# Optimization experiments

Hardware: AMD Instinct MI355X
Metric: run time of the kernel (lower is better)

The kernel has to match this reference:

```python
import jax, jax.numpy as jnp
import numpy as np

HIDDEN = 4096
N_HEADS = 32
N_KV_HEADS = 8
HEAD_DIM = 128
ROPE_BASE = 10000.0


def setup_inputs() -> dict:
    key = jax.random.key(0)
    k1, k2, k3, k4, k5 = jax.random.split(key, 5)
    s = 0.02  # init scale for weights
    return {
        "hidden_states": jax.random.normal(k1, (1, 2048, HIDDEN), dtype=jnp.float32),
        "Wq": jax.random.normal(k2, (N_HEADS * HEAD_DIM, HIDDEN), dtype=jnp.float32) * s,
        "Wk": jax.random.normal(k3, (N_KV_HEADS * HEAD_DIM, HIDDEN), dtype=jnp.float32) * s,
        "Wv": jax.random.normal(k4, (N_KV_HEADS * HEAD_DIM, HIDDEN), dtype=jnp.float32) * s,
        "Wo": jax.random.normal(k5, (HIDDEN, HIDDEN), dtype=jnp.float32) * s,
    }


def _rope(x, cos, sin):
    # x: [B, H, T, D]; cos/sin: [T, D/2] -> rotate split halves (Llama style)
    d2 = x.shape[-1] // 2
    x1, x2 = x[..., :d2], x[..., d2:]
    return jnp.concatenate([x1 * cos - x2 * sin, x1 * sin + x2 * cos], axis=-1)


def reference(hidden_states, Wq, Wk, Wv, Wo):
    B, T, _ = hidden_states.shape
    H, Hkv, D = N_HEADS, N_KV_HEADS, HEAD_DIM
    G = H // Hkv  # kv groups

    q = jnp.einsum("bth,qh->btq", hidden_states, Wq).reshape(B, T, H, D).transpose(0, 2, 1, 3)
    k = jnp.einsum("bth,kh->btk", hidden_states, Wk).reshape(B, T, Hkv, D).transpose(0, 2, 1, 3)
    v = jnp.einsum("bth,vh->btv", hidden_states, Wv).reshape(B, T, Hkv, D).transpose(0, 2, 1, 3)

    # RoPE (position_offset = 0)
    positions = jnp.arange(T, dtype=jnp.float32)
    inv_freq = ROPE_BASE ** (-jnp.arange(0, D, 2, dtype=jnp.float32) / D)  # [D/2]
    angles = positions[:, None] * inv_freq[None, :]                        # [T, D/2]
    cos, sin = jnp.cos(angles), jnp.sin(angles)
    q = _rope(q, cos, sin)
    k = _rope(k, cos, sin)

    # GQA attention without materializing expanded K/V: group query heads
    qg = q.reshape(B, Hkv, G, T, D)
    scale = 1.0 / jnp.sqrt(jnp.asarray(D, dtype=q.dtype))
    scores = jnp.einsum("bkgtd,bksd->bkgts", qg, k) * scale  # [B, Hkv, G, T, T]
    causal = jnp.tril(jnp.ones((T, T), dtype=bool))
    scores = jnp.where(causal, scores, jnp.finfo(scores.dtype).min)
    probs = jax.nn.softmax(scores, axis=-1)
    attn = jnp.einsum("bkgts,bksd->bkgtd", probs, v)          # [B, Hkv, G, T, D]
    attn = attn.reshape(B, H, T, D).transpose(0, 2, 1, 3).reshape(B, T, H * D)

    return jnp.einsum("btq,oq->bto", attn, Wo)
```

## Files before the change

### kernel.cpp

```cpp
#include <hip/hip_runtime.h>
#include <stdint.h>

#define T_SEQ   2048
#define HID     4096
#define NH      32
#define NKV     8
#define HD      128
#define QCOLS   6144
#define QK_SCALE 0.08838834764831845f

typedef _Float16 half_t;
typedef _Float16 half8 __attribute__((ext_vector_type(8)));
typedef _Float16 half4v __attribute__((ext_vector_type(4)));
typedef float    f32x4 __attribute__((ext_vector_type(4)));

typedef __attribute__((address_space(1))) const void cg_void;
typedef __attribute__((address_space(3))) void lds_void;

__global__ __launch_bounds__(256) void cast_all_k(const float* __restrict__ X,
                                                  const float* __restrict__ Wq,
                                                  const float* __restrict__ Wk,
                                                  const float* __restrict__ Wv,
                                                  const float* __restrict__ Wo,
                                                  half_t* __restrict__ Xh,
                                                  half_t* __restrict__ Wqkvh,
                                                  half_t* __restrict__ Woh) {
  int i = blockIdx.x * 256 + threadIdx.x;
  const float* src; half_t* dst; int off;
  if (i < 2097152)      { src = X;  dst = Xh;               off = i; }
  else if (i < 6291456) { src = Wq; dst = Wqkvh;            off = i - 2097152; }
  else if (i < 7340032) { src = Wk; dst = Wqkvh + 16777216; off = i - 6291456; }
  else if (i < 8388608) { src = Wv; dst = Wqkvh + 20971520; off = i - 7340032; }
  else                  { src = Wo; dst = Woh;              off = i - 8388608; }
  f32x4 v = *(const f32x4*)(src + (size_t)off * 4);
  half4v o;
  o[0] = (half_t)v[0]; o[1] = (half_t)v[1]; o[2] = (half_t)v[2]; o[3] = (half_t)v[3];
  *(half4v*)(dst + (size_t)off * 4) = o;
}

__global__ __launch_bounds__(256) void rope_tables_k(float* __restrict__ cs) {
  int idx = blockIdx.x * 256 + threadIdx.x;
  int t = idx >> 6, i = idx & 63;
  float inv = expf(-(float)i * 0.14391156831212787f);
  float a = (float)t * inv;
  cs[idx] = cosf(a);
  cs[131072 + idx] = sinf(a);
}

__global__ __launch_bounds__(256) void rope_vt_k(half_t* __restrict__ QKV,
                                                 const float* __restrict__ cs,
                                                 half_t* __restrict__ Vt) {
  if (blockIdx.x < 20480) {
    int idx = blockIdx.x * 256 + threadIdx.x;
    int i = idx & 63;
    int rem = idx >> 6;
    int head = rem % 40;
    int t = rem / 40;
    int colbase = (head < 32) ? head * HD : HID + (head - 32) * HD;
    size_t base = (size_t)t * QCOLS + colbase;
    float c = cs[t * 64 + i], s = cs[131072 + t * 64 + i];
    float x1 = (float)QKV[base + i];
    float x2 = (float)QKV[base + 64 + i];
    float o1 = x1 * c - x2 * s;
    float o2 = x1 * s + x2 * c;
    if (head < 32) { o1 *= QK_SCALE; o2 *= QK_SCALE; }
    QKV[base + i]      = (half_t)o1;
    QKV[base + 64 + i] = (half_t)o2;
  } else {
    int idx = (blockIdx.x - 20480) * 256 + threadIdx.x;
    int d  = idx & 127;
    int ts = (idx >> 7) & 255;
    int kh = idx >> 15;
    half8 o;
#pragma unroll
    for (int i = 0; i < 8; ++i)
      o[i] = QKV[(size_t)(ts * 8 + i) * QCOLS + HID + NKV * HD + kh * HD + d];
    *(half8*)&Vt[(size_t)kh * (HD * T_SEQ) + (size_t)d * T_SEQ + ts * 8] = o;
  }
}

template <int BM, int BN, int OUT_HALF>
__global__ __launch_bounds__(512, 2) void gemm8p_k(const half_t* __restrict__ A,
                                                   const half_t* __restrict__ Bm,
                                                   void* __restrict__ Cout,
                                                   int M, int N, int K) {
  constexpr int MF = BM / 32;
  constexpr int NF = BN / 64;
  constexpr int MH = MF / 2;
  constexpr int LA = BM / 64;
  constexpr int LB = BN / 64;
  __shared__ half_t Al[2][BM * 64];
  __shared__ half_t Bl[2][BN * 64];

  const int nbm = M / BM;
  const int nwg = nbm * (N / BN);
  const int bid = blockIdx.x;
  const int swz = (bid & 7) * (nwg >> 3) + (bid >> 3);
  const int brow = (swz % nbm) * BM;
  const int bcol = (swz / nbm) * BN;
  const int tid = threadIdx.x;
  const int lane = tid & 63, wid = tid >> 6;
  const int wr = wid >> 2, wc = wid & 3;
  const int lr = lane & 15, hi = lane >> 4;
  const int wrow = wr * (MF * 16), wcol = wc * (NF * 16);

  const half_t* Ab = A + (size_t)brow * K;
  const half_t* Bb = Bm + (size_t)bcol * K;

  f32x4 acc[MF][NF] = {};
  half8 afr[MH], bfr[NF];

#define STAGE_A(l, k0, buf) { \
    int c_ = (l) * 512 + tid; int r_ = c_ >> 3, s_ = c_ & 7; \
    __builtin_amdgcn_global_load_lds( \
      (cg_void*)(Ab + (size_t)r_ * K + (k0) + ((s_ ^ (r_ & 7)) * 8)), \
      (lds_void*)(&Al[buf][((l) * 512 + wid * 64) * 8]), 16, 0, 0); }
#define STAGE_B(l, k0, buf) { \
    int c_ = (l) * 512 + tid; int r_ = c_ >> 3, s_ = c_ & 7; \
    __builtin_amdgcn_global_load_lds( \
      (cg_void*)(Bb + (size_t)r_ * K + (k0) + ((s_ ^ (r_ & 7)) * 8)), \
      (lds_void*)(&Bl[buf][((l) * 512 + wid * 64) * 8]), 16, 0, 0); }
#define RD_A(i, mh, kk, buf) { \
    int row_ = wrow + ((mh) * MH + (i)) * 16 + lr; int ks_ = (kk) * 4 + hi; \
    afr[i] = *(const half8*)&Al[buf][row_ * 64 + ((ks_ ^ (row_ & 7)) * 8)]; }
#define RD_B(n, kk, buf) { \
    int row_ = wcol + (n) * 16 + lr; int ks_ = (kk) * 4 + hi; \
    bfr[n] = *(const half8*)&Bl[buf][row_ * 64 + ((ks_ ^ (row_ & 7)) * 8)]; }
#define MFMA_PH(mh) { \
    __builtin_amdgcn_s_setprio(1); \
    _Pragma("unroll") for (int i_ = 0; i_ < MH; ++i_) \
      _Pragma("unroll") for (int n_ = 0; n_ < NF; ++n_) \
        acc[(mh) * MH + i_][n_] = __builtin_amdgcn_mfma_f32_16x16x32_f16( \
            afr[i_], bfr[n_], acc[(mh) * MH + i_][n_], 0, 0, 0); \
    __builtin_amdgcn_s_setprio(0); }

#define DO_TILE(T, BUF) { \
    const int kn_ = ((T) + 1) * 64; const bool pf_ = ((T) + 1) < NT; \
    if (pf_) { _Pragma("unroll") for (int l_ = 0; l_ < LA; ++l_) STAGE_A(l_, kn_, (BUF) ^ 1); } \
    _Pragma("unroll") for (int n_ = 0; n_ < NF; ++n_) RD_B(n_, 0, BUF); \
    _Pragma("unroll") for (int i_ = 0; i_ < MH; ++i_) RD_A(i_, 0, 0, BUF); \
    MFMA_PH(0); \
    __builtin_amdgcn_s_barrier(); __builtin_amdgcn_sched_barrier(0); \
    if (pf_) { _Pragma("unroll") for (int l_ = 0; l_ < LB; ++l_) STAGE_B(l_, kn_, (BUF) ^ 1); } \
    _Pragma("unroll") for (int i_ = 0; i_ < MH; ++i_) RD_A(i_, 1, 0, BUF); \
    MFMA_PH(1); \
    __builtin_amdgcn_s_barrier(); __builtin_amdgcn_sched_barrier(0); \
    _Pragma("unroll") for (int n_ = 0; n_ < NF; ++n_) RD_B(n_, 1, BUF); \
    _Pragma("unroll") for (int i_ = 0; i_ < MH; ++i_) RD_A(i_, 1, 1, BUF); \
    MFMA_PH(1); \
    __builtin_amdgcn_s_barrier(); __builtin_amdgcn_sched_barrier(0); \
    _Pragma("unroll") for (int i_ = 0; i_ < MH; ++i_) RD_A(i_, 0, 1, BUF); \
    MFMA_PH(0); \
    asm volatile("s_waitcnt vmcnt(0)" ::: "memory"); \
    __syncthreads(); }

  const int NT = K / 64;
#pragma unroll
  for (int l_ = 0; l_ < LA; ++l_) STAGE_A(l_, 0, 0);
#pragma unroll
  for (int l_ = 0; l_ < LB; ++l_) STAGE_B(l_, 0, 0);
  asm volatile("s_waitcnt vmcnt(0)" ::: "memory");
  __syncthreads();

  for (int t = 0; t < NT; t += 2) {
    DO_TILE(t, 0);
    DO_TILE(t + 1, 1);
  }

#undef STAGE_A
#undef STAGE_B
#undef RD_A
#undef RD_B
#undef MFMA_PH
#undef DO_TILE

#pragma unroll
  for (int m = 0; m < MF; ++m)
#pragma unroll
    for (int n = 0; n < NF; ++n)
#pragma unroll
      for (int r = 0; r < 4; ++r) {
        int row = brow + wrow + m * 16 + hi * 4 + r;
        int col = bcol + wcol + n * 16 + lr;
        float v = acc[m][n][r];
        if (OUT_HALF) ((half_t*)Cout)[(size_t)row * N + col] = (half_t)v;
        else          ((float*)Cout)[(size_t)row * N + col] = v;
      }
}

__global__ __launch_bounds__(256, 2) void attn_k(const half_t* __restrict__ QKV,
                                                 const half_t* __restrict__ Vt,
                                                 half_t* __restrict__ Ob) {
  const int bid = blockIdx.x;
  const int qb = 31 - (bid >> 5);
  const int h  = bid & 31;
  const int kh = h >> 2;
  const int tid = threadIdx.x;
  const int lane = tid & 63;
  const int w = tid >> 6;
  const int lr = lane & 15, hi = lane >> 4;
  const int qrow = qb * 64 + w * 16;

  __shared__ half_t Klds[2][64 * 128];
  __shared__ half_t Vlds[2][128 * 64];
  __shared__ half_t Plds[4 * 16 * 72];

  const half_t* Qp  = QKV + h * HD;
  const half_t* Kp  = QKV + HID + kh * HD;
  const half_t* Vtp = Vt + (size_t)kh * (HD * T_SEQ);

  half8 qf[4];
#pragma unroll
  for (int kk = 0; kk < 4; ++kk)
    qf[kk] = *(const half8*)&Qp[(size_t)(qrow + lr) * QCOLS + kk * 32 + hi * 8];

  f32x4 acc[8] = {};
  float mrow[4], lrow[4];
#pragma unroll
  for (int r = 0; r < 4; ++r) { mrow[r] = -1e30f; lrow[r] = 0.0f; }

  half_t* Pw = &Plds[w * (16 * 72)];

#define STAGE_KV(kv0, buf) { \
    _Pragma("unroll") for (int c_ = 0; c_ < 4; ++c_) { \
      int chunk_ = c_ * 256 + tid; \
      int r_ = chunk_ >> 4, s_ = chunk_ & 15; \
      int cc_ = (s_ & 8) | ((s_ ^ r_) & 7); \
      __builtin_amdgcn_global_load_lds( \
          (cg_void*)(Kp + (size_t)((kv0) + r_) * QCOLS + cc_ * 8), \
          (lds_void*)(&Klds[buf][(c_ * 256 + w * 64) * 8]), 16, 0, 0); } \
    _Pragma("unroll") for (int c_ = 0; c_ < 4; ++c_) { \
      int chunk_ = c_ * 256 + tid; \
      int r_ = chunk_ >> 3, s_ = chunk_ & 7; \
      int cc_ = (s_ ^ r_) & 7; \
      __builtin_amdgcn_global_load_lds( \
          (cg_void*)(Vtp + (size_t)r_ * T_SEQ + (kv0) + cc_ * 8), \
          (lds_void*)(&Vlds[buf][(c_ * 256 + w * 64) * 8]), 16, 0, 0); } }

#define COMPUTE(T, BUF) { \
    const int kv0_ = (T) * 64; \
    f32x4 sc[4] = {}; \
    _Pragma("unroll") for (int jt_ = 0; jt_ < 4; ++jt_) \
      _Pragma("unroll") for (int kk_ = 0; kk_ < 4; ++kk_) { \
        int srow_ = jt_ * 16 + lr; \
        int sl_ = kk_ * 4 + hi; \
        int c_ = (sl_ & 8) | ((sl_ ^ srow_) & 7); \
        half8 kf_ = *(const half8*)&Klds[BUF][srow_ * 128 + c_ * 8]; \
        sc[jt_] = __builtin_amdgcn_mfma_f32_16x16x32_f16(qf[kk_], kf_, sc[jt_], 0, 0, 0); \
      } \
    if ((T) == qb) { \
      _Pragma("unroll") for (int jt_ = 0; jt_ < 4; ++jt_) \
        _Pragma("unroll") for (int r_ = 0; r_ < 4; ++r_) { \
          int ig_ = qrow + hi * 4 + r_; \
          int jg_ = kv0_ + jt_ * 16 + lr; \
          if (jg_ > ig_) sc[jt_][r_] = -1e30f; \
        } \
    } \
    float mx_[4]; \
    _Pragma("unroll") for (int r_ = 0; r_ < 4; ++r_) \
      mx_[r_] = fmaxf(fmaxf(sc[0][r_], sc[1][r_]), fmaxf(sc[2][r_], sc[3][r_])); \
    _Pragma("unroll") for (int off_ = 1; off_ < 16; off_ <<= 1) \
      _Pragma("unroll") for (int r_ = 0; r_ < 4; ++r_) \
        mx_[r_] = fmaxf(mx_[r_], __shfl_xor(mx_[r_], off_, 64)); \
    bool grow_ = false; \
    _Pragma("unroll") for (int r_ = 0; r_ < 4; ++r_) grow_ = grow_ || (mx_[r_] > mrow[r_]); \
    if (__any(grow_)) { \
      float scl_[4]; \
      _Pragma("unroll") for (int r_ = 0; r_ < 4; ++r_) { \
        float mn_ = fmaxf(mrow[r_], mx_[r_]); \
        scl_[r_] = __expf(mrow[r_] - mn_); \
        mrow[r_] = mn_; \
        float ls_ = 0.0f; \
        _Pragma("unroll") for (int jt_ = 0; jt_ < 4; ++jt_) { \
          sc[jt_][r_] = __expf(sc[jt_][r_] - mn_); ls_ += sc[jt_][r_]; } \
        lrow[r_] = lrow[r_] * scl_[r_] + ls_; \
      } \
      _Pragma("unroll") for (int g_ = 0; g_ < 8; ++g_) \
        _Pragma("unroll") for (int r_ = 0; r_ < 4; ++r_) acc[g_][r_] *= scl_[r_]; \
    } else { \
      _Pragma("unroll") for (int r_ = 0; r_ < 4; ++r_) { \
        float ls_ = 0.0f; \
        _Pragma("unroll") for (int jt_ = 0; jt_ < 4; ++jt_) { \
          sc[jt_][r_] = __expf(sc[jt_][r_] - mrow[r_]); ls_ += sc[jt_][r_]; } \
        lrow[r_] += ls_; \
      } \
    } \
    _Pragma("unroll") for (int jt_ = 0; jt_ < 4; ++jt_) \
      _Pragma("unroll") for (int r_ = 0; r_ < 4; ++r_) \
        Pw[(hi * 4 + r_) * 72 + jt_ * 16 + lr] = (half_t)sc[jt_][r_]; \
    half8 pf0_ = *(const half8*)&Pw[lr * 72 + hi * 8]; \
    half8 pf1_ = *(const half8*)&Pw[lr * 72 + 32 + hi * 8]; \
    _Pragma("unroll") for (int g_ = 0; g_ < 8; ++g_) { \
      int vrow_ = g_ * 16 + lr; \
      { int c0_ = (hi ^ vrow_) & 7; \
        half8 vf_ = *(const half8*)&Vlds[BUF][vrow_ * 64 + c0_ * 8]; \
        acc[g_] = __builtin_amdgcn_mfma_f32_16x16x32_f16(pf0_, vf_, acc[g_], 0, 0, 0); } \
      { int c1_ = ((4 + hi) ^ vrow_) & 7; \
        half8 vf_ = *(const half8*)&Vlds[BUF][vrow_ * 64 + c1_ * 8]; \
        acc[g_] = __builtin_amdgcn_mfma_f32_16x16x32_f16(pf1_, vf_, acc[g_], 0, 0, 0); } \
    } }

#define TILE_SYNC() { asm volatile("s_waitcnt vmcnt(0)" ::: "memory"); \
                      __builtin_amdgcn_s_barrier(); __builtin_amdgcn_sched_barrier(0); }

  const int nt = qb + 1;
  STAGE_KV(0, 0);
  TILE_SYNC();

  int t = 0;
  for (; t + 2 <= nt; t += 2) {
    STAGE_KV((t + 1) * 64, 1);
    COMPUTE(t, 0);
    TILE_SYNC();
    if (t + 2 < nt) { STAGE_KV((t + 2) * 64, 0); }
    COMPUTE(t + 1, 1);
    TILE_SYNC();
  }
  if (t < nt) { COMPUTE(t, 0); }

#undef STAGE_KV
#undef COMPUTE
#undef TILE_SYNC

  float linv[4];
#pragma unroll
  for (int r = 0; r < 4; ++r) {
    float l = lrow[r];
#pragma unroll
    for (int off = 1; off < 16; off <<= 1) l += __shfl_xor(l, off, 64);
    linv[r] = 1.0f / l;
  }
#pragma unroll
  for (int g = 0; g < 8; ++g)
#pragma unroll
    for (int r = 0; r < 4; ++r) {
      int row = qrow + hi * 4 + r;
      int col = h * HD + g * 16 + lr;
      Ob[(size_t)row * HID + col] = (half_t)(acc[g][r] * linv[r]);
    }
}

extern "C" void kernel_launch(void* const* d_in, const int* in_sizes, int n_in,
                              void* d_out, int out_size, void* d_ws, size_t ws_size,
                              hipStream_t stream) {
  const float* hs = (const float*)d_in[0];
  const float* Wq = (const float*)d_in[1];
  const float* Wk = (const float*)d_in[2];
  const float* Wv = (const float*)d_in[3];
  const float* Wo = (const float*)d_in[4];
  float* out = (float*)d_out;

  char* ws = (char*)d_ws;
  half_t* Xh    = (half_t*)(ws + 0);
  half_t* Vt    = (half_t*)(ws + 0);
  half_t* Wqkvh = (half_t*)(ws + 16777216);
  half_t* Woh   = (half_t*)(ws + 67108864);
  half_t* QKV   = (half_t*)(ws + 100663296);
  half_t* attnh = (half_t*)(ws + 125829120);
  float*  cs    = (float*)(ws + 142606336);
  if (ws_size < 143654912ull) return;

  cast_all_k<<<49152, 256, 0, stream>>>(hs, Wq, Wk, Wv, Wo, Xh, Wqkvh, Woh);
  rope_tables_k<<<512, 256, 0, stream>>>(cs);

  gemm8p_k<256, 192, 1><<<256, 512, 0, stream>>>(Xh, Wqkvh, (void*)QKV, 2048, 6144, 4096);
  rope_vt_k<<<21504, 256, 0, stream>>>(QKV, cs, Vt);
  attn_k<<<1024, 256, 0, stream>>>(QKV, Vt, attnh);
  gemm8p_k<128, 256, 0><<<256, 512, 0, stream>>>(attnh, Woh, (void*)out, 2048, 4096, 4096);
}
```

Baseline: 323.1 us.

## Switch projection GEMMs to 32x32x16 MFMA with new LDS swizzle

Rewrites both projection GEMMs to use 32x32x16 f16 MFMA tiles with configurable wave layout (WM x WN), instead of 16x16x32 tiles. The LDS swizzle is changed to XOR in extra row bits so that the 32-lane-row fragment reads avoid bank conflicts. Larger MFMA tiles need fewer LDS fragment reads per FLOP and fewer instructions. The cost is a larger accumulator register footprint per wave, which could hurt occupancy at 512 threads with two blocks per CU, and a more scattered epilogue store pattern.

Result: slower. 332.3 us (+2.9%).

```diff
diff --git a/kernel.cpp b/kernel.cpp
--- a/kernel.cpp
+++ b/kernel.cpp
@@ -13,6 +13,7 @@
 typedef _Float16 half8 __attribute__((ext_vector_type(8)));
 typedef _Float16 half4v __attribute__((ext_vector_type(4)));
 typedef float    f32x4 __attribute__((ext_vector_type(4)));
+typedef float    f32x16 __attribute__((ext_vector_type(16)));
 
 typedef __attribute__((address_space(1))) const void cg_void;
 typedef __attribute__((address_space(3))) void lds_void;
@@ -79,14 +80,15 @@
   }
 }
 
-template <int BM, int BN, int OUT_HALF>
-__global__ __launch_bounds__(512, 2) void gemm8p_k(const half_t* __restrict__ A,
+#define SWZF(row) (((row) & 7) ^ ((((row) >> 3) & 3) << 1))
+
+template <int BM, int BN, int WM, int WN, int OUT_HALF>
+__global__ __launch_bounds__(512, 2) void gemm32_k(const half_t* __restrict__ A,
                                                    const half_t* __restrict__ Bm,
                                                    void* __restrict__ Cout,
                                                    int M, int N, int K) {
-  constexpr int MF = BM / 32;
-  constexpr int NF = BN / 64;
-  constexpr int MH = MF / 2;
+  constexpr int MR = BM / (WM * 32);
+  constexpr int NR = BN / (WN * 32);
   constexpr int LA = BM / 64;
   constexpr int LB = BN / 64;
   __shared__ half_t Al[2][BM * 64];
@@ -100,57 +102,62 @@
   const int bcol = (swz / nbm) * BN;
   const int tid = threadIdx.x;
   const int lane = tid & 63, wid = tid >> 6;
-  const int wr = wid >> 2, wc = wid & 3;
-  const int lr = lane & 15, hi = lane >> 4;
-  const int wrow = wr * (MF * 16), wcol = wc * (NF * 16);
+  const int wr = wid / WN, wc = wid % WN;
+  const int l32 = lane & 31, h32 = lane >> 5;
+  const int wrow = wr * (MR * 32), wcol = wc * (NR * 32);
 
   const half_t* Ab = A + (size_t)brow * K;
   const half_t* Bb = Bm + (size_t)bcol * K;
 
-  f32x4 acc[MF][NF] = {};
-  half8 afr[MH], bfr[NF];
+  f32x16 acc[MR][NR] = {};
+  half8 afr[MR], bfr[NR];
 
 #define STAGE_A(l, k0, buf) { \
     int c_ = (l) * 512 + tid; int r_ = c_ >> 3, s_ = c_ & 7; \
     __builtin_amdgcn_global_load_lds( \
-      (cg_void*)(Ab + (size_t)r_ * K + (k0) + ((s_ ^ (r_ & 7)) * 8)), \
+      (cg_void*)(Ab + (size_t)r_ * K + (k0) + ((s_ ^ SWZF(r_)) * 8)), \
       (lds_void*)(&Al[buf][((l) * 512 + wid * 64) * 8]), 16, 0, 0); }
 #define STAGE_B(l, k0, buf) { \
     int c_ = (l) * 512 + tid; int r_ = c_ >> 3, s_ = c_ & 7; \
     __builtin_amdgcn_global_load_lds( \
-      (cg_void*)(Bb + (size_t)r_ * K + (k0) + ((s_ ^ (r_ & 7)) * 8)), \
+      (cg_void*)(Bb + (size_t)r_ * K + (k0) + ((s_ ^ SWZF(r_)) * 8)), \
       (lds_void*)(&Bl[buf][((l) * 512 + wid * 64) * 8]), 16, 0, 0); }
-#define RD_A(i, mh, kk, buf) { \
-    int row_ = wrow + ((mh) * MH + (i)) * 16 + lr; int ks_ = (kk) * 4 + hi; \
-    afr[i] = *(const half8*)&Al[buf][row_ * 64 + ((ks_ ^ (row_ & 7)) * 8)]; }
+#define RD_A(m, kk, buf) { \
+    int row_ = wrow + (m) * 32 + l32; int sl_ = ((kk) * 2 + h32) ^ SWZF(row_); \
+    afr[m] = *(const half8*)&Al[buf][row_ * 64 + sl_ * 8]; }
 #define RD_B(n, kk, buf) { \
-    int row_ = wcol + (n) * 16 + lr; int ks_ = (kk) * 4 + hi; \
-    bfr[n] = *(const half8*)&Bl[buf][row_ * 64 + ((ks_ ^ (row_ & 7)) * 8)]; }
-#define MFMA_PH(mh) { \
+    int row_ = wcol + (n) * 32 + l32; int sl_ = ((kk) * 2 + h32) ^ SWZF(row_); \
+    bfr[n] = *(const half8*)&Bl[buf][row_ * 64 + sl_ * 8]; }
+#define MFMA_K() { \
     __builtin_amdgcn_s_setprio(1); \
-    _Pragma("unroll") for (int i_ = 0; i_ < MH; ++i_) \
-      _Pragma("unroll") for (int n_ = 0; n_ < NF; ++n_) \
-        acc[(mh) * MH + i_][n_] = __builtin_amdgcn_mfma_f32_16x16x32_f16( \
-            afr[i_], bfr[n_], acc[(mh) * MH + i_][n_], 0, 0, 0); \
+    _Pragma("unroll") for (int m_ = 0; m_ < MR; ++m_) \
+      _Pragma("unroll") for (int n_ = 0; n_ < NR; ++n_) \
+        acc[m_][n_] = __builtin_amdgcn_mfma_f32_32x32x16_f16( \
+            afr[m_], bfr[n_], acc[m_][n_], 0, 0, 0); \
     __builtin_amdgcn_s_setprio(0); }
+#define RD_ALL(kk, buf) { \
+    _Pragma("unroll") for (int n_ = 0; n_ < NR; ++n_) RD_B(n_, kk, buf); \
+    _Pragma("unroll") for (int m_ = 0; m_ < MR; ++m_) RD_A(m_, kk, buf); }
 
 #define DO_TILE(T, BUF) { \
     const int kn_ = ((T) + 1) * 64; const bool pf_ = ((T) + 1) < NT; \
+     \
     if (pf_) { _Pragma("unroll") for (int l_ = 0; l_ < LA; ++l_) STAGE_A(l_, kn_, (BUF) ^ 1); } \
-    _Pragma("unroll") for (int n_ = 0; n_ < NF; ++n_) RD_B(n_, 0, BUF); \
-    _Pragma("unroll") for (int i_ = 0; i_ < MH; ++i_) RD_A(i_, 0, 0, BUF); \
-    MFMA_PH(0); \
+    RD_ALL(0, BUF); \
+    MFMA_K(); \
     __builtin_amdgcn_s_barrier(); __builtin_amdgcn_sched_barrier(0); \
+     \
     if (pf_) { _Pragma("unroll") for (int l_ = 0; l_ < LB; ++l_) STAGE_B(l_, kn_, (BUF) ^ 1); } \
-    _Pragma("unroll") for (int i_ = 0; i_ < MH; ++i_) RD_A(i_, 1, 0, BUF); \
-    MFMA_PH(1); \
+    RD_ALL(1, BUF); \
+    MFMA_K(); \
     __builtin_amdgcn_s_barrier(); __builtin_amdgcn_sched_barrier(0); \
-    _Pragma("unroll") for (int n_ = 0; n_ < NF; ++n_) RD_B(n_, 1, BUF); \
-    _Pragma("unroll") for (int i_ = 0; i_ < MH; ++i_) RD_A(i_, 1, 1, BUF); \
-    MFMA_PH(1); \
+     \
+    RD_ALL(2, BUF); \
+    MFMA_K(); \
     __builtin_amdgcn_s_barrier(); __builtin_amdgcn_sched_barrier(0); \
-    _Pragma("unroll") for (int i_ = 0; i_ < MH; ++i_) RD_A(i_, 0, 1, BUF); \
-    MFMA_PH(0); \
+     \
+    RD_ALL(3, BUF); \
+    MFMA_K(); \
     asm volatile("s_waitcnt vmcnt(0)" ::: "memory"); \
     __syncthreads(); }
 
@@ -171,17 +178,18 @@
 #undef STAGE_B
 #undef RD_A
 #undef RD_B
-#undef MFMA_PH
+#undef RD_ALL
+#undef MFMA_K
 #undef DO_TILE
 
 #pragma unroll
-  for (int m = 0; m < MF; ++m)
-#pragma unroll
-    for (int n = 0; n < NF; ++n)
-#pragma unroll
-      for (int r = 0; r < 4; ++r) {
-        int row = brow + wrow + m * 16 + hi * 4 + r;
-        int col = bcol + wcol + n * 16 + lr;
+  for (int m = 0; m < MR; ++m)
+#pragma unroll
+    for (int n = 0; n < NR; ++n)
+#pragma unroll
+      for (int r = 0; r < 16; ++r) {
+        int row = brow + wrow + m * 32 + (r & 3) + 8 * (r >> 2) + 4 * h32;
+        int col = bcol + wcol + n * 32 + l32;
         float v = acc[m][n][r];
         if (OUT_HALF) ((half_t*)Cout)[(size_t)row * N + col] = (half_t)v;
         else          ((float*)Cout)[(size_t)row * N + col] = v;
@@ -363,8 +371,8 @@
   cast_all_k<<<49152, 256, 0, stream>>>(hs, Wq, Wk, Wv, Wo, Xh, Wqkvh, Woh);
   rope_tables_k<<<512, 256, 0, stream>>>(cs);
 
-  gemm8p_k<256, 192, 1><<<256, 512, 0, stream>>>(Xh, Wqkvh, (void*)QKV, 2048, 6144, 4096);
+  gemm32_k<256, 192, 4, 2, 1><<<256, 512, 0, stream>>>(Xh, Wqkvh, (void*)QKV, 2048, 6144, 4096);
   rope_vt_k<<<21504, 256, 0, stream>>>(QKV, cs, Vt);
   attn_k<<<1024, 256, 0, stream>>>(QKV, Vt, attnh);
-  gemm8p_k<128, 256, 0><<<256, 512, 0, stream>>>(attnh, Woh, (void*)out, 2048, 4096, 4096);
-}
+  gemm32_k<128, 256, 2, 4, 0><<<256, 512, 0, stream>>>(attnh, Woh, (void*)out, 2048, 4096, 4096);
+}
```
